# Kernel optimization log

Hardware: AMD Instinct MI355X
Metric: run time of the kernel (lower is better)

Reference implementation:

```python
import jax, jax.numpy as jnp
import numpy as np
from functools import partial

# Straight-through sign (Binarize): sign forward, identity gradient
@jax.custom_vjp
def ste_sign(x):
    return jnp.sign(x)

def _ste_fwd(x):
    return jnp.sign(x), None

def _ste_bwd(_, g):
    return (g,)

ste_sign.defvjp(_ste_fwd, _ste_bwd)


def conv2d(x, w):
    # x: [N,C,H,W], w: [O,I,kh,kw], VALID conv, stride 1
    return jax.lax.conv_general_dilated(
        x, w, window_strides=(1, 1), padding='VALID',
        dimension_numbers=('NCHW', 'OIHW', 'NCHW'))


def maxpool2x2(x):
    return jax.lax.reduce_window(
        x, -jnp.inf, jax.lax.max, (1, 1, 2, 2), (1, 1, 2, 2), 'VALID')


def setup_inputs() -> dict:
    key = jax.random.key(0)
    ks = jax.random.split(key, 32)
    d = {}
    d['x'] = jax.random.normal(ks[0], (128, 3, 32, 32), dtype=jnp.float32)
    wshapes = [(128, 3, 3, 3), (128, 128, 3, 3), (256, 128, 3, 3),
               (256, 256, 3, 3), (512, 256, 3, 3), (512, 512, 3, 3),
               (10, 512, 4, 4)]
    for i, s in enumerate(wshapes):
        d[f'w{i+1}'] = jax.random.normal(ks[1 + i], s, dtype=jnp.float32) * 0.05
    bn_ch = [128, 128, 256, 256, 512, 512, 10]
    for i, c in enumerate(bn_ch):
        d[f'bn{i+1}_s'] = jax.random.uniform(ks[10 + 2 * i], (c,), dtype=jnp.float32,
                                             minval=0.5, maxval=1.5)
        d[f'bn{i+1}_t'] = jax.random.normal(ks[11 + 2 * i], (c,), dtype=jnp.float32) * 0.1
    return d


def _forward(x, w1, w2, w3, w4, w5, w6, w7,
             bn1_s, bn1_t, bn2_s, bn2_t, bn3_s, bn3_t, bn4_s, bn4_t,
             bn5_s, bn5_t, bn6_s, bn6_t, bn7_s, bn7_t):
    def block(h, w, s, t, pool, binarize_in):
        if binarize_in:
            h = ste_sign(h)            # binarize activations (in_ch != 3)
        h = jnp.pad(h, ((0, 0), (0, 0), (1, 1), (1, 1)))  # F.pad value=0
        h = conv2d(h, ste_sign(w))      # binarized weights
        if pool:
            h = maxpool2x2(h)
        h = h * s[None, :, None, None] + t[None, :, None, None]  # eval BN
        return jnp.clip(h, -1.0, 1.0)   # Hardtanh

    h = block(x, w1, bn1_s, bn1_t, pool=False, binarize_in=False)  # 32x32x128
    h = block(h, w2, bn2_s, bn2_t, pool=True,  binarize_in=True)   # 16x16x128
    h = block(h, w3, bn3_s, bn3_t, pool=False, binarize_in=True)   # 16x16x256
    h = block(h, w4, bn4_s, bn4_t, pool=True,  binarize_in=True)   # 8x8x256
    h = block(h, w5, bn5_s, bn5_t, pool=False, binarize_in=True)   # 8x8x512
    h = block(h, w6, bn6_s, bn6_t, pool=True,  binarize_in=True)   # 4x4x512
    # conv7: binarize input + weights, 4x4 kernel, no padding -> [N,10,1,1]
    h = conv2d(ste_sign(h), ste_sign(w7))
    h = h.reshape(-1, 10)
    h = h * bn7_s + bn7_t               # eval BatchNorm1d(10)
    return jax.nn.log_softmax(h, axis=1)


def reference(x, w1, w2, w3, w4, w5, w6, w7,
              bn1_s, bn1_t, bn2_s, bn2_t, bn3_s, bn3_t, bn4_s, bn4_t,
              bn5_s, bn5_t, bn6_s, bn6_t, bn7_s, bn7_t):
    return _forward(x, w1, w2, w3, w4, w5, w6, w7,
                    bn1_s, bn1_t, bn2_s, bn2_t, bn3_s, bn3_t, bn4_s, bn4_t,
                    bn5_s, bn5_t, bn6_s, bn6_t, bn7_s, bn7_t)
```

## Files before the change

kernel.cpp:

```cpp
#include <hip/hip_runtime.h>
#include <cstdint>
#include <math.h>

#define NB 128

__global__ void pack_all_kernel(
    const float* __restrict__ w1,
    const float* __restrict__ w2, const float* __restrict__ w3,
    const float* __restrict__ w4, const float* __restrict__ w5,
    const float* __restrict__ w6, const float* __restrict__ w7,
    uint32_t* __restrict__ wp1,
    uint32_t* __restrict__ wp2, uint32_t* __restrict__ wp3,
    uint32_t* __restrict__ wp4, uint32_t* __restrict__ wp5,
    uint32_t* __restrict__ wp6, uint32_t* __restrict__ wp7) {
  int i = blockIdx.x * 256 + threadIdx.x;
  if (i >= 145516) return;
  if (i >= 145408) {
    int j = i - 145408;
    int ocw = j / 27, t = j % 27;
    uint32_t word = 0;
    for (int b = 0; b < 32; ++b)
      word |= ((w1[(ocw * 32 + b) * 27 + t] >= 0.0f) ? 1u : 0u) << b;
    wp1[ocw * 27 + t] = word;
    return;
  }
  const float* w; uint32_t* wp; int C, KHW; bool nl = true;
  if (i < 4608)        { w = w2; wp = wp2; C = 128; KHW = 9; }
  else if (i < 13824)  { i -= 4608;   w = w3; wp = wp3; C = 128; KHW = 9; }
  else if (i < 32256)  { i -= 13824;  w = w4; wp = wp4; C = 256; KHW = 9; }
  else if (i < 69120)  { i -= 32256;  w = w5; wp = wp5; C = 256; KHW = 9; }
  else if (i < 142848) { i -= 69120;  w = w6; wp = wp6; C = 512; KHW = 9; }
  else                 { i -= 142848; w = w7; wp = wp7; C = 512; KHW = 16; nl = false; }
  int Cw = C >> 5;
  int cw = i % Cw;
  int rest = i / Cw;
  int t = rest % KHW;
  int o = rest / KHW;
  uint32_t word = 0;
  for (int b = 0; b < 32; ++b)
    word |= ((w[(o * C + cw * 32 + b) * KHW + t] >= 0.0f) ? 1u : 0u) << b;
  if (nl) wp[(((o >> 6) * KHW + t) * Cw + cw) * 64 + (o & 63)] = word;
  else    wp[(o * KHW + t) * Cw + cw] = word;
}

__device__ __forceinline__ int v_zero() {
  return __builtin_amdgcn_ds_bpermute(0, 0);
}

__global__ __launch_bounds__(256, 2) void conv1_kernel(
    const float* __restrict__ x, const uint32_t* __restrict__ wp1,
    const float* __restrict__ bs, const float* __restrict__ bt,
    uint32_t* __restrict__ out) {
  const int tid = blockIdx.x * 256 + threadIdx.x;
  const int og = blockIdx.y;
  const int px = tid & 31, py = (tid >> 5) & 31, n = tid >> 10;

  float xv[27];
#pragma unroll
  for (int ic = 0; ic < 3; ++ic)
#pragma unroll
    for (int kh = 0; kh < 3; ++kh) {
      const int yy = py + kh - 1;
      const int yc = min(max(yy, 0), 31);
      const float* row = x + ((n * 3 + ic) * 32 + yc) * 32;
#pragma unroll
      for (int kw = 0; kw < 3; ++kw) {
        const int xx = px + kw - 1;
        const int xc = min(max(xx, 0), 31);
        const float v = row[xc];
        const bool ok = ((unsigned)yy < 32u) && ((unsigned)xx < 32u);
        xv[ic * 9 + kh * 3 + kw] = ok ? v : 0.0f;
      }
    }

  uint32_t wout[2];
#pragma unroll
  for (int h = 0; h < 2; ++h) {
    const int ocw = og * 2 + h;
    uint32_t m[27];
#pragma unroll
    for (int t = 0; t < 27; ++t) m[t] = wp1[ocw * 27 + t];
    uint32_t word = 0;
#pragma unroll
    for (int b = 0; b < 32; b += 4) {
      float a0 = 0.f, a1 = 0.f, a2 = 0.f, a3 = 0.f;
#pragma unroll
      for (int t = 0; t < 27; ++t) {
        const uint32_t mt = m[t];
        a0 = fmaf(xv[t], ((mt >> (b + 0)) & 1u) ? 1.0f : -1.0f, a0);
        a1 = fmaf(xv[t], ((mt >> (b + 1)) & 1u) ? 1.0f : -1.0f, a1);
        a2 = fmaf(xv[t], ((mt >> (b + 2)) & 1u) ? 1.0f : -1.0f, a2);
        a3 = fmaf(xv[t], ((mt >> (b + 3)) & 1u) ? 1.0f : -1.0f, a3);
      }
      float aa[4] = {a0, a1, a2, a3};
#pragma unroll
      for (int j = 0; j < 4; ++j) {
        const int oc = ocw * 32 + b + j;
        const float s = bs[oc], t0 = bt[oc];
        const float v = fmaf(aa[j], s, t0);
        bool pos = v >= 0.0f;
        if (fabsf(v) < 1e-3f * s) {
          double ad = 0.0;
          for (int t = 0; t < 27; ++t)
            ad += ((m[t] >> (b + j)) & 1u) ? (double)xv[t] : -(double)xv[t];
          pos = (ad * (double)s + (double)t0) >= 0.0;
        }
        word |= (pos ? 1u : 0u) << (b + j);
      }
    }
    wout[h] = word;
  }
  *(uint64_t*)(out + tid * 4 + og * 2) = ((uint64_t)wout[1] << 32) | wout[0];
}

template <int CW, int CWP, int H, int W, int PC, int R, bool POOL>
__global__ __launch_bounds__(64, 2) void bconv_kernel(
    const uint32_t* __restrict__ act, const uint32_t* __restrict__ wpk,
    const float* __restrict__ bs, const float* __restrict__ bt,
    uint32_t* __restrict__ out, int OCW) {
  static_assert(CW % CWP == 0 && CWP % 4 == 0, "");
  const int lane = threadIdx.x;
  const int ocg = blockIdx.y;
  const int zero = v_zero();
  const int cpr = W / PC;
  const int c = blockIdx.x;
  const int cg = c % cpr;
  const int rg = (c / cpr) % (H / R);
  const int n  = c / (cpr * (H / R));
  const int y0 = rg * R, x0 = cg * PC;

  int acc[R * PC];
#pragma unroll
  for (int p = 0; p < R * PC; ++p) acc[p] = 0;

#pragma unroll
  for (int pass = 0; pass < CW / CWP; ++pass) {
    uint32_t wreg[9 * CWP];
#pragma unroll
    for (int t = 0; t < 9; ++t)
#pragma unroll
      for (int cw = 0; cw < CWP; ++cw)
        wreg[t * CWP + cw] = wpk[(((ocg * 9) + t) * CW + pass * CWP + cw) * 64 + lane];

#pragma unroll
    for (int ry = -1; ry <= R; ++ry) {
      const int y = y0 + ry;
      if (y < 0 || y >= H) continue;
      const uint32_t* rowp = act + zero + (((size_t)n * H + y) * W + x0) * CW + pass * CWP;
      uint32_t buf[(PC + 2) * CWP];
#pragma unroll
      for (int cc = -1; cc <= PC; ++cc) {
        const int x = x0 + cc;
        if (x < 0 || x >= W) continue;
#pragma unroll
        for (int q = 0; q < CWP / 4; ++q)
          *(uint4*)&buf[(cc + 1) * CWP + q * 4] =
              *(const uint4*)(rowp + cc * CW + q * 4);
      }
#pragma unroll
      for (int cc = -1; cc <= PC; ++cc) {
        const int x = x0 + cc;
        if (x < 0 || x >= W) continue;
#pragma unroll
        for (int r = 0; r < R; ++r) {
          const int kh = ry - r + 1;
          if (kh < 0 || kh > 2) continue;
#pragma unroll
          for (int kw = 0; kw < 3; ++kw) {
            const int pxo = cc - kw + 1;
            if (pxo < 0 || pxo >= PC) continue;
#pragma unroll
            for (int cw = 0; cw < CWP; ++cw)
              acc[r * PC + pxo] +=
                  __popc(buf[(cc + 1) * CWP + cw] ^ wreg[(kh * 3 + kw) * CWP + cw]);
          }
        }
      }
    }
  }

  const double sd = (double)bs[ocg * 64 + lane];
  const double td = (double)bt[ocg * 64 + lane];
  if (!POOL) {
    uint64_t bal[R * PC];
#pragma unroll
    for (int r = 0; r < R; ++r)
#pragma unroll
      for (int pxo = 0; pxo < PC; ++pxo) {
        const int y = y0 + r, x = x0 + pxo;
        const int nv = CW * (3 - (y == 0) - (y == H - 1)) * (3 - (x == 0) - (x == W - 1));
        double v = (double)(32 * nv - 2 * acc[r * PC + pxo]) * sd + td;
        bal[r * PC + pxo] = __ballot(v >= 0.0);
      }
    if (lane == 0) {
#pragma unroll
      for (int r = 0; r < R; ++r)
#pragma unroll
        for (int pxo = 0; pxo < PC; ++pxo)
          *(uint64_t*)(out + ((n * H + (y0 + r)) * W + (x0 + pxo)) * OCW + ocg * 2) =
              bal[r * PC + pxo];
    }
  } else {
    static_assert(!POOL || R == 2, "pool needs row pairs");
    uint64_t pooled[PC / 2];
#pragma unroll
    for (int c2 = 0; c2 < PC / 2; ++c2) pooled[c2] = 0;
#pragma unroll
    for (int r = 0; r < R; ++r)
#pragma unroll
      for (int pxo = 0; pxo < PC; ++pxo) {
        const int y = y0 + r, x = x0 + pxo;
        const int nv = CW * (3 - (y == 0) - (y == H - 1)) * (3 - (x == 0) - (x == W - 1));
        double v = (double)(32 * nv - 2 * acc[r * PC + pxo]) * sd + td;
        pooled[pxo >> 1] |= __ballot(v >= 0.0);
      }
    if (lane == 0) {
#pragma unroll
      for (int c2 = 0; c2 < PC / 2; ++c2) {
        const int yo = y0 >> 1, xo = (x0 >> 1) + c2;
        *(uint64_t*)(out + ((n * (H / 2) + yo) * (W / 2) + xo) * OCW + ocg * 2) =
            pooled[c2];
      }
    }
  }
}

__global__ __launch_bounds__(64) void conv7_kernel(
    const uint32_t* __restrict__ act, const uint32_t* __restrict__ wp,
    const float* __restrict__ bs, const float* __restrict__ bt,
    float* __restrict__ out) {
  int n = blockIdx.x;
  int lane = threadIdx.x;
  const uint32_t* a = act + n * 256;
  __shared__ double logits[10];
  for (int o = 0; o < 10; ++o) {
    int acc = 0;
    for (int w = lane; w < 256; w += 64) acc += __popc(a[w] ^ wp[o * 256 + w]);
    for (int off = 32; off > 0; off >>= 1) acc += __shfl_down(acc, off, 64);
    if (lane == 0) {
      double dotd = (double)(8192 - 2 * acc);
      logits[o] = dotd * (double)bs[o] + (double)bt[o];
    }
  }
  __syncthreads();
  if (lane == 0) {
    double m = logits[0];
    for (int o = 1; o < 10; ++o) m = fmax(m, logits[o]);
    double s = 0.0;
    for (int o = 0; o < 10; ++o) s += exp(logits[o] - m);
    double lse = log(s);
    for (int o = 0; o < 10; ++o) out[n * 10 + o] = (float)(logits[o] - m - lse);
  }
}

extern "C" void kernel_launch(void* const* d_in, const int* in_sizes, int n_in,
                              void* d_out, int out_size, void* d_ws, size_t ws_size,
                              hipStream_t stream) {
  const float* x  = (const float*)d_in[0];
  const float* w1 = (const float*)d_in[1];
  const float* w2 = (const float*)d_in[2];
  const float* w3 = (const float*)d_in[3];
  const float* w4 = (const float*)d_in[4];
  const float* w5 = (const float*)d_in[5];
  const float* w6 = (const float*)d_in[6];
  const float* w7 = (const float*)d_in[7];
  const float* s1 = (const float*)d_in[8];  const float* t1 = (const float*)d_in[9];
  const float* s2 = (const float*)d_in[10]; const float* t2 = (const float*)d_in[11];
  const float* s3 = (const float*)d_in[12]; const float* t3 = (const float*)d_in[13];
  const float* s4 = (const float*)d_in[14]; const float* t4 = (const float*)d_in[15];
  const float* s5 = (const float*)d_in[16]; const float* t5 = (const float*)d_in[17];
  const float* s6 = (const float*)d_in[18]; const float* t6 = (const float*)d_in[19];
  const float* s7 = (const float*)d_in[20]; const float* t7 = (const float*)d_in[21];
  float* out = (float*)d_out;

  uint32_t* ws = (uint32_t*)d_ws;
  uint32_t* A   = ws;
  uint32_t* B   = ws + 524288;
  uint32_t* wp2 = ws + 1048576;
  uint32_t* wp3 = wp2 + 4608;
  uint32_t* wp4 = wp3 + 9216;
  uint32_t* wp5 = wp4 + 18432;
  uint32_t* wp6 = wp5 + 36864;
  uint32_t* wp7 = wp6 + 73728;
  uint32_t* wp1 = wp7 + 2560;

  pack_all_kernel<<<dim3(569), dim3(256), 0, stream>>>(
      w1, w2, w3, w4, w5, w6, w7, wp1, wp2, wp3, wp4, wp5, wp6, wp7);

  conv1_kernel<<<dim3(512, 2), dim3(256), 0, stream>>>(x, wp1, s1, t1, A);

  bconv_kernel<4, 4, 32, 32, 8, 2, true>
      <<<dim3(8192, 2), dim3(64), 0, stream>>>(A, wp2, s2, t2, B, 4);

  bconv_kernel<4, 4, 16, 16, 8, 1, false>
      <<<dim3(4096, 4), dim3(64), 0, stream>>>(B, wp3, s3, t3, A, 8);

  bconv_kernel<8, 4, 16, 16, 8, 2, true>
      <<<dim3(2048, 4), dim3(64), 0, stream>>>(A, wp4, s4, t4, B, 8);

  bconv_kernel<8, 4, 8, 8, 8, 2, false>
      <<<dim3(512, 8), dim3(64), 0, stream>>>(B, wp5, s5, t5, A, 16);

  bconv_kernel<16, 4, 8, 8, 8, 2, true>
      <<<dim3(512, 8), dim3(64), 0, stream>>>(A, wp6, s6, t6, B, 16);

  conv7_kernel<<<dim3(128), dim3(64), 0, stream>>>(B, wp7, s7, t7, out);
}
```

Before: 322.3 us.

## Precompute integer BN-sign thresholds and shrink conv tiles for higher occupancy

The pack kernel now also computes, for each output channel, the smallest integer dot product d with d*s+t >= 0. The binary conv epilogue then uses an integer compare on the popcount, replacing double-precision FMA per pixel. Pixel tiles per wave drop from 8 to 4 columns, with grids doubled and launch bounds raised to 4 waves per SIMD, giving more parallelism and lower register pressure. The exchange is reloading more halo and weights per tile, plus reliance on the exact integer threshold search, which only scans a small window around -t/s.

Measured after the change: 318.6 us. Within noise of the previous version (-1.1%).

```diff
diff --git a/kernel.cpp b/kernel.cpp
--- a/kernel.cpp
+++ b/kernel.cpp
@@ -9,12 +9,34 @@
     const float* __restrict__ w2, const float* __restrict__ w3,
     const float* __restrict__ w4, const float* __restrict__ w5,
     const float* __restrict__ w6, const float* __restrict__ w7,
+    const float* __restrict__ s2, const float* __restrict__ t2,
+    const float* __restrict__ s3, const float* __restrict__ t3,
+    const float* __restrict__ s4, const float* __restrict__ t4,
+    const float* __restrict__ s5, const float* __restrict__ t5,
+    const float* __restrict__ s6, const float* __restrict__ t6,
     uint32_t* __restrict__ wp1,
     uint32_t* __restrict__ wp2, uint32_t* __restrict__ wp3,
     uint32_t* __restrict__ wp4, uint32_t* __restrict__ wp5,
-    uint32_t* __restrict__ wp6, uint32_t* __restrict__ wp7) {
+    uint32_t* __restrict__ wp6, uint32_t* __restrict__ wp7,
+    int* __restrict__ thr) {
   int i = blockIdx.x * 256 + threadIdx.x;
-  if (i >= 145516) return;
+  if (i >= 147180) return;
+  if (i >= 145516) {
+    int j = i - 145516;
+    const float *bsp, *btp; int idx;
+    if (j < 128)       { bsp = s2; btp = t2; idx = j; }
+    else if (j < 384)  { bsp = s3; btp = t3; idx = j - 128; }
+    else if (j < 640)  { bsp = s4; btp = t4; idx = j - 384; }
+    else if (j < 1152) { bsp = s5; btp = t5; idx = j - 640; }
+    else               { bsp = s6; btp = t6; idx = j - 1152; }
+    const double s = (double)bsp[idx], t = (double)btp[idx];
+    int d0 = (int)floor(-t / s);
+    int th = d0 + 4;
+    for (int d = d0 - 3; d <= d0 + 4; ++d)
+      if ((double)d * s + t >= 0.0) { th = d; break; }
+    thr[j] = th;
+    return;
+  }
   if (i >= 145408) {
     int j = i - 145408;
     int ocw = j / 27, t = j % 27;
@@ -114,9 +136,9 @@
 }
 
 template <int CW, int CWP, int H, int W, int PC, int R, bool POOL>
-__global__ __launch_bounds__(64, 2) void bconv_kernel(
+__global__ __launch_bounds__(64, 4) void bconv_kernel(
     const uint32_t* __restrict__ act, const uint32_t* __restrict__ wpk,
-    const float* __restrict__ bs, const float* __restrict__ bt,
+    const int* __restrict__ thrp,
     uint32_t* __restrict__ out, int OCW) {
   static_assert(CW % CWP == 0 && CWP % 4 == 0, "");
   const int lane = threadIdx.x;
@@ -129,6 +151,8 @@
   const int n  = c / (cpr * (H / R));
   const int y0 = rg * R, x0 = cg * PC;
 
+  const int thr = thrp[ocg * 64 + lane];
+
   int acc[R * PC];
 #pragma unroll
   for (int p = 0; p < R * PC; ++p) acc[p] = 0;
@@ -179,8 +203,6 @@
     }
   }
 
-  const double sd = (double)bs[ocg * 64 + lane];
-  const double td = (double)bt[ocg * 64 + lane];
   if (!POOL) {
     uint64_t bal[R * PC];
 #pragma unroll
@@ -188,9 +210,9 @@
 #pragma unroll
       for (int pxo = 0; pxo < PC; ++pxo) {
         const int y = y0 + r, x = x0 + pxo;
-        const int nv = CW * (3 - (y == 0) - (y == H - 1)) * (3 - (x == 0) - (x == W - 1));
-        double v = (double)(32 * nv - 2 * acc[r * PC + pxo]) * sd + td;
-        bal[r * PC + pxo] = __ballot(v >= 0.0);
+        const int nv32 =
+            32 * CW * (3 - (y == 0) - (y == H - 1)) * (3 - (x == 0) - (x == W - 1));
+        bal[r * PC + pxo] = __ballot(acc[r * PC + pxo] <= ((nv32 - thr) >> 1));
       }
     if (lane == 0) {
 #pragma unroll
@@ -210,9 +232,9 @@
 #pragma unroll
       for (int pxo = 0; pxo < PC; ++pxo) {
         const int y = y0 + r, x = x0 + pxo;
-        const int nv = CW * (3 - (y == 0) - (y == H - 1)) * (3 - (x == 0) - (x == W - 1));
-        double v = (double)(32 * nv - 2 * acc[r * PC + pxo]) * sd + td;
-        pooled[pxo >> 1] |= __ballot(v >= 0.0);
+        const int nv32 =
+            32 * CW * (3 - (y == 0) - (y == H - 1)) * (3 - (x == 0) - (x == W - 1));
+        pooled[pxo >> 1] |= __ballot(acc[r * PC + pxo] <= ((nv32 - thr) >> 1));
       }
     if (lane == 0) {
 #pragma unroll
@@ -283,26 +305,29 @@
   uint32_t* wp6 = wp5 + 36864;
   uint32_t* wp7 = wp6 + 73728;
   uint32_t* wp1 = wp7 + 2560;
-
-  pack_all_kernel<<<dim3(569), dim3(256), 0, stream>>>(
-      w1, w2, w3, w4, w5, w6, w7, wp1, wp2, wp3, wp4, wp5, wp6, wp7);
+  int* thr      = (int*)(wp1 + 108);
+
+  pack_all_kernel<<<dim3(575), dim3(256), 0, stream>>>(
+      w1, w2, w3, w4, w5, w6, w7,
+      s2, t2, s3, t3, s4, t4, s5, t5, s6, t6,
+      wp1, wp2, wp3, wp4, wp5, wp6, wp7, thr);
 
   conv1_kernel<<<dim3(512, 2), dim3(256), 0, stream>>>(x, wp1, s1, t1, A);
 
-  bconv_kernel<4, 4, 32, 32, 8, 2, true>
-      <<<dim3(8192, 2), dim3(64), 0, stream>>>(A, wp2, s2, t2, B, 4);
-
-  bconv_kernel<4, 4, 16, 16, 8, 1, false>
-      <<<dim3(4096, 4), dim3(64), 0, stream>>>(B, wp3, s3, t3, A, 8);
-
-  bconv_kernel<8, 4, 16, 16, 8, 2, true>
-      <<<dim3(2048, 4), dim3(64), 0, stream>>>(A, wp4, s4, t4, B, 8);
-
-  bconv_kernel<8, 4, 8, 8, 8, 2, false>
-      <<<dim3(512, 8), dim3(64), 0, stream>>>(B, wp5, s5, t5, A, 16);
-
-  bconv_kernel<16, 4, 8, 8, 8, 2, true>
-      <<<dim3(512, 8), dim3(64), 0, stream>>>(A, wp6, s6, t6, B, 16);
+  bconv_kernel<4, 4, 32, 32, 4, 2, true>
+      <<<dim3(16384, 2), dim3(64), 0, stream>>>(A, wp2, thr + 0, B, 4);
+
+  bconv_kernel<4, 4, 16, 16, 4, 2, false>
+      <<<dim3(4096, 4), dim3(64), 0, stream>>>(B, wp3, thr + 128, A, 8);
+
+  bconv_kernel<8, 4, 16, 16, 4, 2, true>
+      <<<dim3(4096, 4), dim3(64), 0, stream>>>(A, wp4, thr + 384, B, 8);
+
+  bconv_kernel<8, 4, 8, 8, 4, 2, false>
+      <<<dim3(1024, 8), dim3(64), 0, stream>>>(B, wp5, thr + 640, A, 16);
+
+  bconv_kernel<16, 4, 8, 8, 4, 2, true>
+      <<<dim3(1024, 8), dim3(64), 0, stream>>>(A, wp6, thr + 1152, B, 16);
 
   conv7_kernel<<<dim3(128), dim3(64), 0, stream>>>(B, wp7, s7, t7, out);
 }
```
